# Optimization experiments

Measured on AMD Instinct MI355X. Metric: run time of the kernel, lower is better.

The kernel has to match this reference:

```python
import jax, jax.numpy as jnp
import numpy as np

B = 131072
D_IN = 256
HID = 256
N_EXPERTS = 4
N_IN_CAPS = 1
CAP_DIM = 16
BN_EPS = 1e-5


def setup_inputs() -> dict:
    key = jax.random.key(0)
    ks = jax.random.split(key, 8)
    return {
        "x": jax.random.normal(ks[0], (B, D_IN), dtype=jnp.float32),
        "fc_w": jax.random.normal(ks[1], (HID, D_IN), dtype=jnp.float32) * (1.0 / np.sqrt(D_IN)),
        "fc_b": jax.random.normal(ks[2], (HID,), dtype=jnp.float32) * 0.01,
        "bn_gamma": jnp.ones((HID,), dtype=jnp.float32),
        "bn_beta": jnp.zeros((HID,), dtype=jnp.float32),
        "W_caps": jax.random.normal(ks[3], (N_EXPERTS, N_IN_CAPS, HID, CAP_DIM), dtype=jnp.float32),
        "out_w": jax.random.normal(ks[4], (N_EXPERTS, CAP_DIM), dtype=jnp.float32) * (1.0 / np.sqrt(CAP_DIM)),
        "out_b": jax.random.normal(ks[5], (N_EXPERTS,), dtype=jnp.float32) * 0.01,
    }


def _squash(v):
    # norm/(1+norm^2) * v/(norm+1e-8), norm over last axis
    norm = jnp.linalg.norm(v, axis=-1, keepdims=True)
    return (norm / (1.0 + norm * norm)) * (v / (norm + 1e-8))


def reference(x, fc_w, fc_b, bn_gamma, bn_beta, W_caps, out_w, out_b):
    # Linear 256->256
    h = x @ fc_w.T + fc_b                                   # [B, HID]
    # BatchNorm1d (training-mode batch statistics, biased variance)
    mean = jnp.mean(h, axis=0)
    var = jnp.mean(jnp.square(h - mean), axis=0)
    h = (h - mean) * jax.lax.rsqrt(var + BN_EPS) * bn_gamma + bn_beta
    h = jax.nn.relu(h)
    # Capsule layer: input capsules [B, N_IN, HID]
    x_cap = h[:, None, :]                                   # [B, 1, HID]
    # u[b,e,n,o] = sum_d x_cap[b,n,d] * W_caps[e,n,d,o]
    u = jnp.einsum('bnd,endo->beno', x_cap, W_caps)         # [B, E, 1, 16]
    u_hat = _squash(u)
    # dynamic routing, 3 iterations
    b = jnp.zeros((x.shape[0], N_EXPERTS, N_IN_CAPS), dtype=h.dtype)
    v = None
    for i in range(3):
        c = jax.nn.softmax(b, axis=1)                       # over experts
        s = jnp.sum(c[..., None] * u_hat, axis=2)           # [B, E, 16]
        v = _squash(s)
        if i < 2:
            b = b + jnp.sum(u_hat * v[:, :, None, :], axis=-1)
    # output head + softmax
    logits = jnp.einsum('bec,kc->bek', v, out_w) + out_b    # [B, E, E]
    return jax.nn.softmax(logits, axis=-1)
```

## Files before the change

kernel.cpp:

```cpp
#include <hip/hip_runtime.h>
#include <hip/hip_bf16.h>


#define BATCH   131072
#define INV_B   (1.0f / 131072.0f)

typedef __attribute__((ext_vector_type(8))) short  short8;
typedef __attribute__((ext_vector_type(4))) float  f32x4;

__device__ __forceinline__ unsigned bf16_rn(float f) {
    unsigned u = __float_as_uint(f);
    return (u + 0x7fffu + ((u >> 16) & 1u)) >> 16;
}

__device__ __forceinline__ void split8(const float* v, uint4& hi, uint4& lo) {
    unsigned hb[8], lb[8];
#pragma unroll
    for (int j = 0; j < 8; ++j) {
        union { __hip_bfloat16 b; ushort u; } ch, cl;
        ch.b = __float2bfloat16(v[j]);
        float res = v[j] - __bfloat162float(ch.b);
        cl.b = __float2bfloat16(res);
        hb[j] = ch.u;
        lb[j] = cl.u;
    }
    hi = make_uint4(hb[0] | (hb[1] << 16), hb[2] | (hb[3] << 16),
                    hb[4] | (hb[5] << 16), hb[6] | (hb[7] << 16));
    lo = make_uint4(lb[0] | (lb[1] << 16), lb[2] | (lb[3] << 16),
                    lb[4] | (lb[5] << 16), lb[6] | (lb[7] << 16));
}

__device__ __forceinline__ uint4 cvt8(const float* v) {
    unsigned hb[8];
#pragma unroll
    for (int j = 0; j < 8; ++j) {
        union { __hip_bfloat16 b; ushort u; } ch;
        ch.b = __float2bfloat16(v[j]);
        hb[j] = ch.u;
    }
    return make_uint4(hb[0] | (hb[1] << 16), hb[2] | (hb[3] << 16),
                      hb[4] | (hb[5] << 16), hb[6] | (hb[7] << 16));
}

__global__ void k_prep(const float* __restrict__ w, ushort* __restrict__ wsp,
                       float* __restrict__ gsum, float* __restrict__ gsq)
{
    if (blockIdx.x == 0) { gsum[threadIdx.x] = 0.f; gsq[threadIdx.x] = 0.f; }
    const int cid = (int)blockIdx.x * 256 + threadIdx.x;
    const int j   = cid >> 5;
    const int ks  = (cid >> 2) & 7;
    const int c   = cid & 3;
    const float* wp = w + j * 256 + ks * 32 + c * 8;
    float4 v0 = *(const float4*)(wp);
    float4 v1 = *(const float4*)(wp + 4);
    float va[8] = {v0.x, v0.y, v0.z, v0.w, v1.x, v1.y, v1.z, v1.w};
    uint4 hi, lo;
    split8(va, hi, lo);
    const int slot = (c + (j >> 1)) & 3;
    *(uint4*)&wsp[ks * 8192 + j * 32 + slot * 8]         = hi;
    *(uint4*)&wsp[65536 + ks * 8192 + j * 32 + slot * 8] = lo;
}

__global__ __launch_bounds__(256, 3) void k_gemm(
    const float* __restrict__ x, const ushort* __restrict__ wsp,
    const float* __restrict__ bias, ushort* __restrict__ h,
    float* __restrict__ gsum, float* __restrict__ gsq)
{
    __shared__ ushort Ah[128 * 32];
    __shared__ ushort Bh[2][128 * 32];
    __shared__ ushort Bl[2][128 * 32];
    __shared__ float  csum[128];
    __shared__ float  csq[128];

    const int t   = threadIdx.x;
    const int wid = t >> 6;
    const int l   = t & 63;
    const int wm  = wid >> 1;
    const int wn  = wid & 1;
    const int g   = l >> 4;
    const int lc  = l & 15;

    const int wg = ((int)blockIdx.x & 7) * 256 + ((int)blockIdx.x >> 3);
    const int bm = (wg >> 1) * 128;
    const int bn = (wg & 1) * 128;

    if (t < 128) { csum[t] = 0.f; csq[t] = 0.f; }

    f32x4 acc[4][4];
#pragma unroll
    for (int mi = 0; mi < 4; ++mi)
#pragma unroll
        for (int ni = 0; ni < 4; ++ni)
            acc[mi][ni] = (f32x4){0.f, 0.f, 0.f, 0.f};

    float bb[4];
#pragma unroll
    for (int ni = 0; ni < 4; ++ni)
        bb[ni] = bias[bn + wn * 64 + ni * 16 + lc];

    const int ar  = t >> 1;
    const int ac0 = (t & 1) * 2;
    const int as0 = (ac0 + (ar >> 1)) & 3;
    const int as1 = (ac0 + 1 + (ar >> 1)) & 3;
    const float* aptr = x + (size_t)(bm + ar) * 256 + ac0 * 8;

    float4 v0, v1, v2, v3;
    v0 = *(const float4*)(aptr);
    v1 = *(const float4*)(aptr + 4);
    v2 = *(const float4*)(aptr + 8);
    v3 = *(const float4*)(aptr + 12);
    {
        const char* srch = (const char*)(wsp + bn * 32);
        const char* srcl = (const char*)(wsp + 65536 + bn * 32);
#pragma unroll
        for (int i = 0; i < 2; ++i) {
            const int off = wid * 2048 + i * 1024;
            __builtin_amdgcn_global_load_lds(
                (const __attribute__((address_space(1))) unsigned*)(srch + off + l * 16),
                (__attribute__((address_space(3))) unsigned*)((char*)Bh[0] + off),
                16, 0, 0);
            __builtin_amdgcn_global_load_lds(
                (const __attribute__((address_space(1))) unsigned*)(srcl + off + l * 16),
                (__attribute__((address_space(3))) unsigned*)((char*)Bl[0] + off),
                16, 0, 0);
        }
    }
    {
        float va[8] = {v0.x, v0.y, v0.z, v0.w, v1.x, v1.y, v1.z, v1.w};
        float vb[8] = {v2.x, v2.y, v2.z, v2.w, v3.x, v3.y, v3.z, v3.w};
        *(uint4*)&Ah[ar * 32 + as0 * 8] = cvt8(va);
        *(uint4*)&Ah[ar * 32 + as1 * 8] = cvt8(vb);
    }

    int cur = 0;
#pragma unroll 1
    for (int ks = 0; ks < 8; ++ks) {
        __syncthreads();

        if (ks < 7) {
            const float* ap = aptr + (ks + 1) * 32;
            v0 = *(const float4*)(ap);
            v1 = *(const float4*)(ap + 4);
            v2 = *(const float4*)(ap + 8);
            v3 = *(const float4*)(ap + 12);
            const char* srch = (const char*)(wsp + (ks + 1) * 8192 + bn * 32);
            const char* srcl = (const char*)(wsp + 65536 + (ks + 1) * 8192 + bn * 32);
            char* dsth = (char*)Bh[cur ^ 1];
            char* dstl = (char*)Bl[cur ^ 1];
#pragma unroll
            for (int i = 0; i < 2; ++i) {
                const int off = wid * 2048 + i * 1024;
                __builtin_amdgcn_global_load_lds(
                    (const __attribute__((address_space(1))) unsigned*)(srch + off + l * 16),
                    (__attribute__((address_space(3))) unsigned*)(dsth + off),
                    16, 0, 0);
                __builtin_amdgcn_global_load_lds(
                    (const __attribute__((address_space(1))) unsigned*)(srcl + off + l * 16),
                    (__attribute__((address_space(3))) unsigned*)(dstl + off),
                    16, 0, 0);
            }
        }

        {
            short8 ahf[4];
#pragma unroll
            for (int mi = 0; mi < 4; ++mi) {
                const int row = wm * 64 + mi * 16 + lc;
                const int off = row * 32 + ((g + (row >> 1)) & 3) * 8;
                ahf[mi] = *(const short8*)&Ah[off];
            }
#pragma unroll
            for (int ni = 0; ni < 4; ++ni) {
                const int col = wn * 64 + ni * 16 + lc;
                const int off = col * 32 + ((g + (col >> 1)) & 3) * 8;
                short8 bhf = *(const short8*)&Bh[cur][off];
                short8 blf = *(const short8*)&Bl[cur][off];
#pragma unroll
                for (int mi = 0; mi < 4; ++mi) {
                    acc[mi][ni] = __builtin_amdgcn_mfma_f32_16x16x32_bf16(
                        ahf[mi], bhf, acc[mi][ni], 0, 0, 0);
                    acc[mi][ni] = __builtin_amdgcn_mfma_f32_16x16x32_bf16(
                        ahf[mi], blf, acc[mi][ni], 0, 0, 0);
                }
            }
        }
        __syncthreads();

        if (ks < 7) {
            float va[8] = {v0.x, v0.y, v0.z, v0.w, v1.x, v1.y, v1.z, v1.w};
            float vb[8] = {v2.x, v2.y, v2.z, v2.w, v3.x, v3.y, v3.z, v3.w};
            *(uint4*)&Ah[ar * 32 + as0 * 8] = cvt8(va);
            *(uint4*)&Ah[ar * 32 + as1 * 8] = cvt8(vb);
        }
        cur ^= 1;
    }

    float lsum[4] = {0.f, 0.f, 0.f, 0.f};
    float lsq[4]  = {0.f, 0.f, 0.f, 0.f};

#pragma unroll
    for (int mi = 0; mi < 4; ++mi)
#pragma unroll
        for (int ni = 0; ni < 4; ++ni) {
            const int colg = bn + wn * 64 + ni * 16 + lc;
#pragma unroll
            for (int reg = 0; reg < 4; ++reg) {
                const int row = bm + wm * 64 + mi * 16 + g * 4 + reg;
                float hv = acc[mi][ni][reg] + bb[ni];
                unsigned hb = bf16_rn(hv);
                float hq = __uint_as_float(hb << 16);
                h[(size_t)row * 256 + colg] = (ushort)hb;
                lsum[ni] += hq;
                lsq[ni]   = fmaf(hq, hq, lsq[ni]);
            }
        }

#pragma unroll
    for (int ni = 0; ni < 4; ++ni) {
        lsum[ni] += __shfl_xor(lsum[ni], 16);
        lsum[ni] += __shfl_xor(lsum[ni], 32);
        lsq[ni]  += __shfl_xor(lsq[ni], 16);
        lsq[ni]  += __shfl_xor(lsq[ni], 32);
    }
    if (l < 16) {
#pragma unroll
        for (int ni = 0; ni < 4; ++ni) {
            atomicAdd(&csum[wn * 64 + ni * 16 + lc], lsum[ni]);
            atomicAdd(&csq[wn * 64 + ni * 16 + lc],  lsq[ni]);
        }
    }
    __syncthreads();
    if (t < 128) {
        atomicAdd(&gsum[bn + t], csum[t]);
        atomicAdd(&gsq[bn + t],  csq[t]);
    }
}

__global__ __launch_bounds__(256) void k_fuse(
    const ushort* __restrict__ h,
    const float* __restrict__ gsum, const float* __restrict__ gsq,
    const float* __restrict__ gamma, const float* __restrict__ beta,
    const float* __restrict__ wc, const float* __restrict__ ow_g,
    const float* __restrict__ ob_g, float* __restrict__ out)
{
    __shared__ ushort Hh[32 * 256];
    __shared__ ushort Hl[32 * 256];
    __shared__ float  us[64 * 68];
    __shared__ float  ows[64];
    __shared__ float  abs_[512];

    const int t   = threadIdx.x;
    const int wid = t >> 6;
    const int l   = t & 63;
    const int g   = l >> 4;
    const int lc  = l & 15;

    {
        float mean = gsum[t] * INV_B;
        float var  = gsq[t] * INV_B - mean * mean;
        float rstd = rsqrtf(var + 1e-5f);
        float a = gamma[t] * rstd;
        abs_[t]       = a;
        abs_[256 + t] = beta[t] - mean * a;
    }
    if (t < 64) ows[t] = ow_g[t];

    short8 afh[8], afl[8];
#pragma unroll
    for (int ks = 0; ks < 8; ++ks) {
        union { ushort u16[8]; short8 v; } ph, pl;
#pragma unroll
        for (int j = 0; j < 8; ++j) {
            const int d = ks * 32 + g * 8 + j;
            float wv = wc[wid * 4096 + d * 16 + lc];
            unsigned hh = bf16_rn(wv);
            float res = wv - __uint_as_float(hh << 16);
            ph.u16[j] = (ushort)hh;
            pl.u16[j] = (ushort)bf16_rn(res);
        }
        afh[ks] = ph.v;
        afl[ks] = pl.v;
    }
    __syncthreads();

    const int c8 = (t & 31) * 8;
    float a_[8], cj[8];
    {
        float4 x0 = *(const float4*)(abs_ + c8);
        float4 x1 = *(const float4*)(abs_ + c8 + 4);
        float4 y0 = *(const float4*)(abs_ + 256 + c8);
        float4 y1 = *(const float4*)(abs_ + 256 + c8 + 4);
        a_[0]=x0.x; a_[1]=x0.y; a_[2]=x0.z; a_[3]=x0.w;
        a_[4]=x1.x; a_[5]=x1.y; a_[6]=x1.z; a_[7]=x1.w;
        cj[0]=y0.x; cj[1]=y0.y; cj[2]=y0.z; cj[3]=y0.w;
        cj[4]=y1.x; cj[5]=y1.y; cj[6]=y1.z; cj[7]=y1.w;
    }

    const int rowBase = (int)blockIdx.x * 64;

#pragma unroll
    for (int sub = 0; sub < 2; ++sub) {
        const int row0 = rowBase + sub * 32;

        __syncthreads();

#pragma unroll
        for (int it = 0; it < 4; ++it) {
            const int r = it * 8 + (t >> 5);
            const ushort* hp = h + (size_t)(row0 + r) * 256 + c8;
            short8 hraw = *(const short8*)hp;
            float hv[8];
#pragma unroll
            for (int j = 0; j < 8; ++j) {
                unsigned ub = (unsigned)(ushort)hraw[j];
                hv[j] = __uint_as_float(ub << 16);
                hv[j] = fmaxf(fmaf(hv[j], a_[j], cj[j]), 0.f);
            }
            uint4 hi, lo;
            split8(hv, hi, lo);
            const int slot = (t & 31) ^ (r & 7);
            *(uint4*)&Hh[r * 256 + slot * 8] = hi;
            *(uint4*)&Hl[r * 256 + slot * 8] = lo;
        }
        __syncthreads();

        f32x4 acc0 = (f32x4){0.f,0.f,0.f,0.f};
        f32x4 acc1 = (f32x4){0.f,0.f,0.f,0.f};
#pragma unroll
        for (int ks = 0; ks < 8; ++ks) {
            {
                const int row  = lc;
                const int slot = (ks * 4 + g) ^ (row & 7);
                short8 bh = *(const short8*)&Hh[row * 256 + slot * 8];
                short8 bl = *(const short8*)&Hl[row * 256 + slot * 8];
                acc0 = __builtin_amdgcn_mfma_f32_16x16x32_bf16(afh[ks], bh, acc0, 0,0,0);
                acc0 = __builtin_amdgcn_mfma_f32_16x16x32_bf16(afh[ks], bl, acc0, 0,0,0);
                acc0 = __builtin_amdgcn_mfma_f32_16x16x32_bf16(afl[ks], bh, acc0, 0,0,0);
            }
            {
                const int row  = 16 + lc;
                const int slot = (ks * 4 + g) ^ (row & 7);
                short8 bh = *(const short8*)&Hh[row * 256 + slot * 8];
                short8 bl = *(const short8*)&Hl[row * 256 + slot * 8];
                acc1 = __builtin_amdgcn_mfma_f32_16x16x32_bf16(afh[ks], bh, acc1, 0,0,0);
                acc1 = __builtin_amdgcn_mfma_f32_16x16x32_bf16(afh[ks], bl, acc1, 0,0,0);
                acc1 = __builtin_amdgcn_mfma_f32_16x16x32_bf16(afl[ks], bh, acc1, 0,0,0);
            }
        }
        {
            const int r0 = sub * 32 + lc;
            *(float4*)&us[r0 * 68 + wid * 16 + g * 4] =
                make_float4(acc0[0], acc0[1], acc0[2], acc0[3]);
            *(float4*)&us[(r0 + 16) * 68 + wid * 16 + g * 4] =
                make_float4(acc1[0], acc1[1], acc1[2], acc1[3]);
        }
    }
    __syncthreads();

    const int row_l = wid * 16 + lc;
    float u[16];
#pragma unroll
    for (int q = 0; q < 4; ++q) {
        float4 v4 = *(const float4*)&us[row_l * 68 + g * 16 + q * 4];
        u[q*4+0] = v4.x; u[q*4+1] = v4.y; u[q*4+2] = v4.z; u[q*4+3] = v4.w;
    }

    float n2 = 0.f;
#pragma unroll
    for (int o = 0; o < 16; ++o) n2 = fmaf(u[o], u[o], n2);
    const float nrm = sqrtf(n2);
    const float sc  = nrm / ((1.f + n2) * (nrm + 1e-8f));
    const float nh2 = sc * sc * n2;
    const float nh  = sc * nrm;

    float tk[4];
#pragma unroll
    for (int k = 0; k < 4; ++k) {
        float s = 0.f;
#pragma unroll
        for (int q = 0; q < 4; ++q) {
            float4 w4 = *(const float4*)&ows[k * 16 + q * 4];
            s = fmaf(u[q*4+0], w4.x, s);
            s = fmaf(u[q*4+1], w4.y, s);
            s = fmaf(u[q*4+2], w4.z, s);
            s = fmaf(u[q*4+3], w4.w, s);
        }
        tk[k] = s;
    }

    float b = 0.f, alc = 0.f;
#pragma unroll
    for (int it3 = 0; it3 < 3; ++it3) {
        float bmax = fmaxf(b, __shfl_xor(b, 16));
        bmax = fmaxf(bmax, __shfl_xor(bmax, 32));
        float eb = __expf(b - bmax);
        float es = eb + __shfl_xor(eb, 16);
        es += __shfl_xor(es, 32);
        float c = eb / es;
        float ns  = c * nh;
        float ns2 = c * c * nh2;
        float av  = ns / ((1.f + ns2) * (ns + 1e-8f));
        alc = av * c;
        if (it3 < 2) b += alc * nh2;
    }

    const float vs = alc * sc;
    float p0 = fmaf(vs, tk[0], ob_g[0]);
    float p1 = fmaf(vs, tk[1], ob_g[1]);
    float p2 = fmaf(vs, tk[2], ob_g[2]);
    float p3 = fmaf(vs, tk[3], ob_g[3]);
    float mx = fmaxf(fmaxf(p0, p1), fmaxf(p2, p3));
    float e0 = __expf(p0 - mx), e1 = __expf(p1 - mx);
    float e2 = __expf(p2 - mx), e3 = __expf(p3 - mx);
    float inv = 1.f / (e0 + e1 + e2 + e3);
    *(float4*)&out[(size_t)(rowBase + row_l) * 16 + g * 4] =
        make_float4(e0 * inv, e1 * inv, e2 * inv, e3 * inv);
}

extern "C" void kernel_launch(void* const* d_in, const int* in_sizes, int n_in,
                              void* d_out, int out_size, void* d_ws, size_t ws_size,
                              hipStream_t stream)
{
    const float* x     = (const float*)d_in[0];
    const float* fc_w  = (const float*)d_in[1];
    const float* fc_b  = (const float*)d_in[2];
    const float* gamma = (const float*)d_in[3];
    const float* beta  = (const float*)d_in[4];
    const float* wc    = (const float*)d_in[5];
    const float* ow    = (const float*)d_in[6];
    const float* ob    = (const float*)d_in[7];
    float* out = (float*)d_out;

    float*  gsum = (float*)d_ws;
    float*  gsq  = gsum + 256;
    ushort* h    = (ushort*)((char*)d_ws + 4096);

    ushort* wsp = (ushort*)d_out;

    k_prep <<<dim3(32),   dim3(256), 0, stream>>>(fc_w, wsp, gsum, gsq);
    k_gemm <<<dim3(2048), dim3(256), 0, stream>>>(x, wsp, fc_b, h, gsum, gsq);
    k_fuse <<<dim3(2048), dim3(256), 0, stream>>>(h, gsum, gsq, gamma, beta,
                                                  wc, ow, ob, out);
}
```

Measured before the change: 103.8 us.

## Double-buffer A tile and make each wave stage its own B half with one barrier

```diff
diff --git a/kernel.cpp b/kernel.cpp
--- a/kernel.cpp
+++ b/kernel.cpp
@@ -66,9 +66,9 @@
     const float* __restrict__ bias, ushort* __restrict__ h,
     float* __restrict__ gsum, float* __restrict__ gsq)
 {
-    __shared__ ushort Ah[128 * 32];
-    __shared__ ushort Bh[2][128 * 32];
-    __shared__ ushort Bl[2][128 * 32];
+    __shared__ ushort Ah[2][128 * 32];
+    __shared__ ushort Bhs[2][128 * 32];
+    __shared__ ushort Bls[2][128 * 32];
     __shared__ float  csum[128];
     __shared__ float  csq[128];
 
@@ -104,62 +104,55 @@
     const int as1 = (ac0 + 1 + (ar >> 1)) & 3;
     const float* aptr = x + (size_t)(bm + ar) * 256 + ac0 * 8;
 
-    float4 v0, v1, v2, v3;
-    v0 = *(const float4*)(aptr);
-    v1 = *(const float4*)(aptr + 4);
-    v2 = *(const float4*)(aptr + 8);
-    v3 = *(const float4*)(aptr + 12);
-    {
-        const char* srch = (const char*)(wsp + bn * 32);
-        const char* srcl = (const char*)(wsp + 65536 + bn * 32);
-#pragma unroll
-        for (int i = 0; i < 2; ++i) {
-            const int off = wid * 2048 + i * 1024;
-            __builtin_amdgcn_global_load_lds(
-                (const __attribute__((address_space(1))) unsigned*)(srch + off + l * 16),
-                (__attribute__((address_space(3))) unsigned*)((char*)Bh[0] + off),
-                16, 0, 0);
-            __builtin_amdgcn_global_load_lds(
-                (const __attribute__((address_space(1))) unsigned*)(srcl + off + l * 16),
-                (__attribute__((address_space(3))) unsigned*)((char*)Bl[0] + off),
-                16, 0, 0);
-        }
-    }
+    const size_t bsrc0 = (size_t)(bn + wn * 64) * 32;
+
+#define STAGE_B(KS, BUF)                                                      \
+    {                                                                         \
+        const char* sh_ = (const char*)(wsp + (KS) * 8192 + bsrc0);           \
+        const char* sl_ = (const char*)(wsp + 65536 + (KS) * 8192 + bsrc0);   \
+        char* dh_ = (char*)Bhs[BUF] + wn * 4096;                              \
+        char* dl_ = (char*)Bls[BUF] + wn * 4096;                              \
+        _Pragma("unroll")                                                     \
+        for (int i_ = 0; i_ < 4; ++i_) {                                      \
+            __builtin_amdgcn_global_load_lds(                                 \
+                (const __attribute__((address_space(1))) unsigned*)(sh_ + i_ * 1024 + l * 16), \
+                (__attribute__((address_space(3))) unsigned*)(dh_ + i_ * 1024), 16, 0, 0); \
+            __builtin_amdgcn_global_load_lds(                                 \
+                (const __attribute__((address_space(1))) unsigned*)(sl_ + i_ * 1024 + l * 16), \
+                (__attribute__((address_space(3))) unsigned*)(dl_ + i_ * 1024), 16, 0, 0); \
+        }                                                                     \
+    }
+
+    float4 v0 = *(const float4*)(aptr);
+    float4 v1 = *(const float4*)(aptr + 4);
+    float4 v2 = *(const float4*)(aptr + 8);
+    float4 v3 = *(const float4*)(aptr + 12);
+    STAGE_B(0, 0)
+    asm volatile("s_waitcnt vmcnt(0)" ::: "memory");
     {
         float va[8] = {v0.x, v0.y, v0.z, v0.w, v1.x, v1.y, v1.z, v1.w};
         float vb[8] = {v2.x, v2.y, v2.z, v2.w, v3.x, v3.y, v3.z, v3.w};
-        *(uint4*)&Ah[ar * 32 + as0 * 8] = cvt8(va);
-        *(uint4*)&Ah[ar * 32 + as1 * 8] = cvt8(vb);
-    }
+        *(uint4*)&Ah[0][ar * 32 + as0 * 8] = cvt8(va);
+        *(uint4*)&Ah[0][ar * 32 + as1 * 8] = cvt8(vb);
+    }
+    asm volatile("s_waitcnt lgkmcnt(0)" ::: "memory");
+    __builtin_amdgcn_s_barrier();
 
     int cur = 0;
 #pragma unroll 1
     for (int ks = 0; ks < 8; ++ks) {
-        __syncthreads();
-
         if (ks < 7) {
             const float* ap = aptr + (ks + 1) * 32;
             v0 = *(const float4*)(ap);
             v1 = *(const float4*)(ap + 4);
             v2 = *(const float4*)(ap + 8);
             v3 = *(const float4*)(ap + 12);
-            const char* srch = (const char*)(wsp + (ks + 1) * 8192 + bn * 32);
-            const char* srcl = (const char*)(wsp + 65536 + (ks + 1) * 8192 + bn * 32);
-            char* dsth = (char*)Bh[cur ^ 1];
-            char* dstl = (char*)Bl[cur ^ 1];
-#pragma unroll
-            for (int i = 0; i < 2; ++i) {
-                const int off = wid * 2048 + i * 1024;
-                __builtin_amdgcn_global_load_lds(
-                    (const __attribute__((address_space(1))) unsigned*)(srch + off + l * 16),
-                    (__attribute__((address_space(3))) unsigned*)(dsth + off),
-                    16, 0, 0);
-                __builtin_amdgcn_global_load_lds(
-                    (const __attribute__((address_space(1))) unsigned*)(srcl + off + l * 16),
-                    (__attribute__((address_space(3))) unsigned*)(dstl + off),
-                    16, 0, 0);
-            }
-        }
+            STAGE_B(ks + 1, cur ^ 1)
+            asm volatile("s_waitcnt vmcnt(12)" ::: "memory");
+        } else {
+            asm volatile("s_waitcnt vmcnt(0)" ::: "memory");
+        }
+        __builtin_amdgcn_sched_barrier(0);
 
         {
             short8 ahf[4];
@@ -167,14 +160,14 @@
             for (int mi = 0; mi < 4; ++mi) {
                 const int row = wm * 64 + mi * 16 + lc;
                 const int off = row * 32 + ((g + (row >> 1)) & 3) * 8;
-                ahf[mi] = *(const short8*)&Ah[off];
+                ahf[mi] = *(const short8*)&Ah[cur][off];
             }
 #pragma unroll
             for (int ni = 0; ni < 4; ++ni) {
                 const int col = wn * 64 + ni * 16 + lc;
                 const int off = col * 32 + ((g + (col >> 1)) & 3) * 8;
-                short8 bhf = *(const short8*)&Bh[cur][off];
-                short8 blf = *(const short8*)&Bl[cur][off];
+                short8 bhf = *(const short8*)&Bhs[cur][off];
+                short8 blf = *(const short8*)&Bls[cur][off];
 #pragma unroll
                 for (int mi = 0; mi < 4; ++mi) {
                     acc[mi][ni] = __builtin_amdgcn_mfma_f32_16x16x32_bf16(
@@ -184,16 +177,20 @@
                 }
             }
         }
-        __syncthreads();
 
         if (ks < 7) {
+            asm volatile("s_waitcnt vmcnt(8)" ::: "memory");
+            __builtin_amdgcn_sched_barrier(0);
             float va[8] = {v0.x, v0.y, v0.z, v0.w, v1.x, v1.y, v1.z, v1.w};
             float vb[8] = {v2.x, v2.y, v2.z, v2.w, v3.x, v3.y, v3.z, v3.w};
-            *(uint4*)&Ah[ar * 32 + as0 * 8] = cvt8(va);
-            *(uint4*)&Ah[ar * 32 + as1 * 8] = cvt8(vb);
+            *(uint4*)&Ah[cur ^ 1][ar * 32 + as0 * 8] = cvt8(va);
+            *(uint4*)&Ah[cur ^ 1][ar * 32 + as1 * 8] = cvt8(vb);
+            asm volatile("s_waitcnt lgkmcnt(0)" ::: "memory");
+            __builtin_amdgcn_s_barrier();
         }
         cur ^= 1;
     }
+#undef STAGE_B
 
     float lsum[4] = {0.f, 0.f, 0.f, 0.f};
     float lsq[4]  = {0.f, 0.f, 0.f, 0.f};
```

New measurement: 104.4 us. About the same (+0.6%).
